# Optimization experiments

Hardware: AMD Instinct MI355X
Metric: run time of the kernel (lower is better)

## Reference

```python
import jax, jax.numpy as jnp
import numpy as np

DEPTH, HEADS, DIM_HEAD = 6, 8, 64
B, N, E = 2, 128, 160
NUM_ATOMS, NF = 100, 127
DIM = NF + 1                 # 128, node feature dim fed to transformer
INNER = HEADS * DIM_HEAD     # 512


def setup_inputs() -> dict:
    key = jax.random.key(0)
    ks = iter(jax.random.split(key, 40))
    f32 = jnp.float32
    def w(shape, scale=0.02):
        return jax.random.normal(next(ks), shape, dtype=f32) * scale
    inp = {
        "indices": jax.random.randint(next(ks), (B, N), 0, NUM_ATOMS),
        "coordinates": jax.random.normal(next(ks), (B, N, 3), dtype=f32),
        "bonds": jax.random.randint(next(ks), (E, 2), 0, N),
        "noise_level": jax.random.uniform(next(ks), (1,), dtype=f32),
        "atom_emb": w((NUM_ATOMS, NF), 1.0),
        "ln1_g": jnp.ones((DEPTH, DIM), f32), "ln1_b": jnp.zeros((DEPTH, DIM), f32),
        "Wq": w((DEPTH, DIM, INNER)), "bq": jnp.zeros((DEPTH, INNER), f32),
        "Wkv": w((DEPTH, DIM, 2 * INNER)), "bkv": jnp.zeros((DEPTH, 2 * INNER), f32),
        "We": w((DEPTH, 3, INNER)), "be": jnp.zeros((DEPTH, INNER), f32),
        "Wo": w((DEPTH, INNER, DIM)), "bo": jnp.zeros((DEPTH, DIM), f32),
        "Wg1": w((DEPTH, 3 * DIM, 1)),
        "ln2_g": jnp.ones((DEPTH, DIM), f32), "ln2_b": jnp.zeros((DEPTH, DIM), f32),
        "W1": w((DEPTH, DIM, 4 * DIM)), "b1": jnp.zeros((DEPTH, 4 * DIM), f32),
        "W2": w((DEPTH, 4 * DIM, DIM)), "b2": jnp.zeros((DEPTH, DIM), f32),
        "Wg2": w((DEPTH, 3 * DIM, 1)),
        "Wlin": w((DIM, 1)), "blin": jnp.zeros((1,), f32),
    }
    return inp


def _ln(x, g, b, eps=1e-5):
    m = jnp.mean(x, -1, keepdims=True)
    v = jnp.mean((x - m) ** 2, -1, keepdims=True)
    return (x - m) * jax.lax.rsqrt(v + eps) * g + b


def _gated_residual(x, res, Wg):
    # gate = sigmoid(Linear([x, res, x-res])); out = x*gate + res*(1-gate)
    gate = jax.nn.sigmoid(jnp.concatenate([x, res, x - res], -1) @ Wg)  # (B,N,1)
    return x * gate + res * (1.0 - gate)


def _forward(indices, bonds, coordinates, noise_level, atom_emb,
             ln1_g, ln1_b, Wq, bq, Wkv, bkv, We, be, Wo, bo, Wg1,
             ln2_g, ln2_b, W1, b1, W2, b2, Wg2, Wlin, blin):
    b, n = indices.shape
    # nodes_embedding: atom embedding + noise-level channel
    noise = jnp.broadcast_to(noise_level.reshape(1, 1, 1).astype(coordinates.dtype), (b, n, 1))
    nodes = jnp.concatenate([atom_emb[indices], noise], -1)  # (B,N,DIM)
    # edges_embedding: vectorized scatter of per-bond coordinate differences
    i, j = bonds[:, 0], bonds[:, 1]
    diff = coordinates[:, i] - coordinates[:, j]             # (B,E,3)
    edges = jnp.zeros((b, n, n, 3), coordinates.dtype)
    edges = edges.at[:, i, j].set(diff).at[:, j, i].set(-diff)

    scale = DIM_HEAD ** -0.5
    for l in range(DEPTH):
        # PreNorm + edge-biased attention (mask is all-ones -> no-op)
        xn = _ln(nodes, ln1_g[l], ln1_b[l])
        q = (xn @ Wq[l] + bq[l]).reshape(b, n, HEADS, DIM_HEAD)
        k, v = jnp.split(xn @ Wkv[l] + bkv[l], 2, -1)
        k = k.reshape(b, n, HEADS, DIM_HEAD)
        v = v.reshape(b, n, HEADS, DIM_HEAD)
        e = (edges @ We[l] + be[l]).reshape(b, n, n, HEADS, DIM_HEAD)
        kk = k[:, None] + e                                   # (B,i,j,H,D)
        vv = v[:, None] + e
        sim = jnp.einsum('bihd,bijhd->bijh', q, kk) * scale
        attn = jax.nn.softmax(sim, axis=2)                    # softmax over j
        out = jnp.einsum('bijh,bijhd->bihd', attn, vv).reshape(b, n, INNER)
        out = out @ Wo[l] + bo[l]
        nodes = _gated_residual(out, nodes, Wg1[l])
        # PreNorm + FeedForward (exact GELU, mult=4) + gated residual
        xn = _ln(nodes, ln2_g[l], ln2_b[l])
        ff = jax.nn.gelu(xn @ W1[l] + b1[l], approximate=False) @ W2[l] + b2[l]
        nodes = _gated_residual(ff, nodes, Wg2[l])
    return jnp.sum(nodes @ Wlin + blin)


def reference(indices, coordinates, bonds, noise_level, atom_emb,
              ln1_g, ln1_b, Wq, bq, Wkv, bkv, We, be, Wo, bo, Wg1,
              ln2_g, ln2_b, W1, b1, W2, b2, Wg2, Wlin, blin):
    return _forward(indices, bonds, coordinates, noise_level, atom_emb,
                    ln1_g, ln1_b, Wq, bq, Wkv, bkv, We, be, Wo, bo, Wg1,
                    ln2_g, ln2_b, W1, b1, W2, b2, Wg2, Wlin, blin)
```

## Files before the change

### kernel.cpp

```cpp
#include <hip/hip_runtime.h>
#include <hip/hip_fp16.h>
#include <math.h>

#define DEPTH 6
#define NN    128
#define EE    160
#define NF    127
#define DIMM  128
#define INNER 512
#define NNODE 256

typedef _Float16 h2f16 __attribute__((ext_vector_type(2)));

#if defined(__has_builtin)
#if __has_builtin(__builtin_amdgcn_fdot2)
#define HAVE_FDOT2 1
#endif
#endif

__device__ __forceinline__ float fdot2f(h2f16 a, h2f16 b, float c) {
#ifdef HAVE_FDOT2
    return __builtin_amdgcn_fdot2(a, b, c, false);
#else
    return c + (float)a.x * (float)b.x + (float)a.y * (float)b.y;
#endif
}

__device__ __forceinline__ void gload16(const void* g, void* l) {
    __builtin_amdgcn_global_load_lds((const __attribute__((address_space(1))) void*)g,
                                     (__attribute__((address_space(3))) void*)l,
                                     16, 0, 0);
}

template <int N>
__device__ __forceinline__ void wait_vm() {
    __builtin_amdgcn_s_waitcnt((0xF << 8) | (7 << 4) | (N & 0xF) | ((N >> 4) << 14));
}
__device__ __forceinline__ void wait_lgkm0() { __builtin_amdgcn_s_waitcnt(0xC07F); }
__device__ __forceinline__ void sbar0() { __builtin_amdgcn_sched_barrier(0); }

__device__ __forceinline__ void stage8c(const char* g, char* lds, int ln) {
#pragma unroll
    for (int i = 0; i < 8; i++)
        gload16(g + i * 1024 + ln * 16, lds + i * 1024);
}
__device__ __forceinline__ void stage8f(const char* g, int rs, char* lds, int ln) {
#pragma unroll
    for (int i = 0; i < 8; i++)
        gload16(g + (size_t)i * rs + ln * 16, lds + i * 1024);
}


template <int NXT>
__device__ __forceinline__ float gemv512v2(const __half* s_xh, float* wbuf,
                                           const char* nextG, int ln) {
    const char* Wb = (const char*)wbuf;
    float4 wa[8], wb[8];
    wait_vm<8>();
#pragma unroll
    for (int i = 0; i < 8; i++) wa[i] = *(const float4*)(Wb + i * 1024 + ln * 16);
    sbar0(); wait_lgkm0(); sbar0();
    if (NXT) { stage8c(nextG, (char*)wbuf, ln); wait_vm<8>(); }
    else     wait_vm<0>();
#pragma unroll
    for (int i = 0; i < 8; i++) wb[i] = *(const float4*)(Wb + 8192 + i * 1024 + ln * 16);
    sbar0(); wait_lgkm0(); sbar0();
    if (NXT) stage8c(nextG + 8192, (char*)wbuf + 8192, ln);
    const float4* X = (const float4*)s_xh;
    float a0 = 0, a1 = 0, a2 = 0, a3 = 0;
#pragma unroll
    for (int i = 0; i < 8; i++) {
        float4 xv = X[i];
        const h2f16* wh = (const h2f16*)&wa[i];
        const h2f16* xh = (const h2f16*)&xv;
        a0 = fdot2f(xh[0], wh[0], a0); a1 = fdot2f(xh[1], wh[1], a1);
        a2 = fdot2f(xh[2], wh[2], a2); a3 = fdot2f(xh[3], wh[3], a3);
    }
#pragma unroll
    for (int i = 0; i < 8; i++) {
        float4 xv = X[8 + i];
        const h2f16* wh = (const h2f16*)&wb[i];
        const h2f16* xh = (const h2f16*)&xv;
        a0 = fdot2f(xh[0], wh[0], a0); a1 = fdot2f(xh[1], wh[1], a1);
        a2 = fdot2f(xh[2], wh[2], a2); a3 = fdot2f(xh[3], wh[3], a3);
    }
    return (a0 + a1) + (a2 + a3);
}

template <int NXT>
__device__ __forceinline__ float gemv128v2(const __half* s_xp, float* wbuf,
                                           const char* nextG, int ln) {
    const char* Wb = (const char*)wbuf;
    const char* Xb = (const char*)s_xp + (ln & 3) * 272;
    float4 wa[8], wb[8];
    wait_vm<8>();
#pragma unroll
    for (int i = 0; i < 8; i++) wa[i] = *(const float4*)(Wb + i * 1024 + ln * 16);
    sbar0(); wait_lgkm0(); sbar0();
    if (NXT) { stage8c(nextG, (char*)wbuf, ln); wait_vm<8>(); }
    else     wait_vm<0>();
#pragma unroll
    for (int i = 0; i < 8; i++) wb[i] = *(const float4*)(Wb + 8192 + i * 1024 + ln * 16);
    sbar0(); wait_lgkm0(); sbar0();
    if (NXT) stage8c(nextG + 8192, (char*)wbuf + 8192, ln);
    float a0 = 0, a1 = 0, a2 = 0, a3 = 0;
#pragma unroll
    for (int i = 0; i < 8; i++) {
        float4 xv = *(const float4*)(Xb + i * 16);
        const h2f16* wh = (const h2f16*)&wa[i];
        const h2f16* xh = (const h2f16*)&xv;
        a0 = fdot2f(xh[0], wh[0], a0); a1 = fdot2f(xh[1], wh[1], a1);
        a2 = fdot2f(xh[2], wh[2], a2); a3 = fdot2f(xh[3], wh[3], a3);
    }
#pragma unroll
    for (int i = 0; i < 8; i++) {
        float4 xv = *(const float4*)(Xb + 128 + i * 16);
        const h2f16* wh = (const h2f16*)&wb[i];
        const h2f16* xh = (const h2f16*)&xv;
        a0 = fdot2f(xh[0], wh[0], a0); a1 = fdot2f(xh[1], wh[1], a1);
        a2 = fdot2f(xh[2], wh[2], a2); a3 = fdot2f(xh[3], wh[3], a3);
    }
    return (a0 + a1) + (a2 + a3);
}

template <int NXT>
__device__ __forceinline__ float4 gemvf32(const float* s_xn, float* wbuf,
                                          const char* nextG, int nrs, int w, int ln) {
    const float4* w4 = (const float4*)wbuf;
    float4 wr[16];
    wait_vm<8>();
#pragma unroll
    for (int r = 0; r < 8; r++) wr[r] = w4[r * 64 + ln];
    sbar0(); wait_lgkm0(); sbar0();
    if (NXT) { stage8f(nextG, nrs, (char*)wbuf, ln); wait_vm<8>(); }
    else     wait_vm<0>();
#pragma unroll
    for (int r = 8; r < 16; r++) wr[r] = w4[r * 64 + ln];
    sbar0(); wait_lgkm0(); sbar0();
    if (NXT) stage8f(nextG + (size_t)8 * nrs, nrs, (char*)wbuf + 8192, ln);
    float4 acc = {0, 0, 0, 0};
#pragma unroll
    for (int r = 0; r < 16; r++) {
        float a = s_xn[w * 16 + r];
        acc.x += a * wr[r].x; acc.y += a * wr[r].y;
        acc.z += a * wr[r].z; acc.w += a * wr[r].w;
    }
    return acc;
}

template <int N>
__device__ __forceinline__ void block_reduce_n(float* vals, float* sbuf) {
#pragma unroll
    for (int off = 32; off > 0; off >>= 1)
#pragma unroll
        for (int q = 0; q < N; q++) vals[q] += __shfl_xor(vals[q], off, 64);
    int wave = threadIdx.x >> 6;
    if ((threadIdx.x & 63) == 0)
#pragma unroll
        for (int q = 0; q < N; q++) sbuf[wave * N + q] = vals[q];
    __syncthreads();
#pragma unroll
    for (int q = 0; q < N; q++) {
        float r = 0.0f;
#pragma unroll
        for (int g = 0; g < 8; g++) r += sbuf[g * N + q];
        vals[q] = r;
    }
    __syncthreads();
}

__device__ __forceinline__ float gelu_exact(float a) {
    return 0.5f * a * (1.0f + erff(a * 0.70710678f));
}

__global__ __launch_bounds__(512, 1) void k_pre(
        const int* indices, const float* coords, const int* bonds, const float* noise,
        const float* atom_emb, const float* ln1_g, const float* ln1_b,
        const float* Wq, const float* bq, const float* Wkv, const float* bkv,
        const float* Wo, const float* W1, const float* W2,
        __half* hWq, __half* hWkv, __half* hWo, __half* hW1, __half* hW2,
        float* nodes, float* qb, __half* hk, __half* hv, float* sedgews,
        const float* blin, float* out) {
    int bn = blockIdx.x;
    int b = bn >> 7, i = bn & 127;
    int t  = threadIdx.x;
    int d  = t & 127;
    bool own = (t < 128);
    int w = t >> 6, ln = t & 63;
    __shared__ float arena[32768];
    __shared__ float scoord[384];
    __shared__ int   sadj[128];
    __shared__ float s_xn[128];
    __shared__ float s_red[48];
    __shared__ float s_part[2048];
    float* wbuf = arena + w * 4096;
    char*  wbufc = (char*)wbuf;

    if (bn == 0 && t == 0) out[0] = 256.0f * blin[0];

    const char* phB[6] = {(const char*)Wq,            (const char*)Wq + 1024,
                          (const char*)Wkv,           (const char*)Wkv + 1024,
                          (const char*)Wkv + 2048,    (const char*)Wkv + 3072};
    const int phRS[6] = {2048, 2048, 4096, 4096, 4096, 4096};

    stage8f(phB[0] + (size_t)(w * 16) * phRS[0], phRS[0], wbufc, ln);
    stage8f(phB[0] + (size_t)(w * 16 + 8) * phRS[0], phRS[0], wbufc + 8192, ln);

    if (t < 3 * NN) scoord[t] = coords[b * 3 * NN + t];
    if (t < NN) sadj[t] = 0;
    __syncthreads();
    if (t < EE) {
        int e0 = bonds[2 * t], e1 = bonds[2 * t + 1];
        if (e0 == i) sadj[e1] = 1;
        if (e1 == i) sadj[e0] = 1;
    }
    __syncthreads();
    if (t < NN) {
        int j = t;
        float msk = sadj[j] ? 1.0f : 0.0f;
        sedgews[bn * 384 + 3 * j + 0] = msk * (scoord[3 * i + 0] - scoord[3 * j + 0]);
        sedgews[bn * 384 + 3 * j + 1] = msk * (scoord[3 * i + 1] - scoord[3 * j + 1]);
        sedgews[bn * 384 + 3 * j + 2] = msk * (scoord[3 * i + 2] - scoord[3 * j + 2]);
    }

    float nd = 0.0f;
    if (own) {
        int idx = indices[bn];
        nd = (d < NF) ? atom_emb[idx * NF + d] : noise[0];
        nodes[bn * DIMM + d] = nd;
    }
    {
        float vals[2] = {own ? nd : 0.0f, own ? nd * nd : 0.0f};
        block_reduce_n<2>(vals, s_red);
        float m   = vals[0] * (1.0f / 128.0f);
        float var = vals[1] * (1.0f / 128.0f) - m * m;
        if (own) s_xn[d] = (nd - m) * rsqrtf(var + 1e-5f) * ln1_g[d] + ln1_b[d];
    }

    for (int u = bn * 512 + t; u < 294912; u += NNODE * 512) {
        int s = u >> 13, within = u & 8191;
        int l = s / 6, m = s % 6;
        const float* src; __half* dst; int ncols, colofs, big;
        if (m == 0)      { src = Wq  + (size_t)l * 65536;  dst = hWq  + (size_t)l * 65536;         ncols = 512;  colofs = 0;   big = 0; }
        else if (m == 1) { src = Wkv + (size_t)l * 131072; dst = hWkv + (size_t)l * 131072;        ncols = 1024; colofs = 0;   big = 0; }
        else if (m == 2) { src = Wkv + (size_t)l * 131072; dst = hWkv + (size_t)l * 131072 + 65536;ncols = 1024; colofs = 512; big = 0; }
        else if (m == 3) { src = W1  + (size_t)l * 65536;  dst = hW1  + (size_t)l * 65536;         ncols = 512;  colofs = 0;   big = 0; }
        else if (m == 4) { src = Wo  + (size_t)l * 65536;  dst = hWo  + (size_t)l * 65536;         ncols = 128;  colofs = 0;   big = 1; }
        else             { src = W2  + (size_t)l * 65536;  dst = hW2  + (size_t)l * 65536;         ncols = 128;  colofs = 0;   big = 1; }
        int rb, col;
        if (!big) { rb = within >> 9; col = within & 511; }
        else      { rb = within >> 7; col = within & 127; }
        int row0 = rb * 8;
        __align__(16) __half tmp[8];
#pragma unroll
        for (int e = 0; e < 8; e++)
            tmp[e] = __float2half(src[(size_t)(row0 + e) * ncols + colofs + col]);
        int dh;
        if (!big) dh = (col >> 6) * 8192 + rb * 512 + (col & 63) * 8;
        else {
            int kq = row0 >> 7, ci = (row0 & 127) >> 3;
            dh = (col >> 4) * 8192 + ci * 512 + ((col & 15) * 4 + kq) * 8;
        }
        *(float4*)&dst[dh] = *(const float4*)tmp;
    }
    __syncthreads();

#define PRE_COMBINE(P)                                                        \
    {                                                                         \
        ((float4*)(s_part + w * 256))[ln] = acc;                              \
        __syncthreads();                                                      \
        if (t < 256) {                                                        \
            float sS = 0.0f;                                                  \
            _Pragma("unroll")                                                 \
            for (int g = 0; g < 8; g++) sS += s_part[g * 256 + t];            \
            int col = ((P) & 1) * 256 + t;                                    \
            if ((P) < 2)      qb[(size_t)bn * INNER + col] = sS + bq[col];    \
            else if ((P) < 4) hk[(size_t)bn * INNER + col] =                  \
                                  __float2half(sS + bkv[col]);                \
            else              hv[(size_t)bn * INNER + col] =                  \
                                  __float2half(sS + bkv[INNER + col]);        \
        }                                                                     \
        __syncthreads();                                                      \
    }

    {
        float4 acc;
        acc = gemvf32<1>(s_xn, wbuf, phB[1] + (size_t)(w * 16) * phRS[1], phRS[1], w, ln);
        PRE_COMBINE(0);
        acc = gemvf32<1>(s_xn, wbuf, phB[2] + (size_t)(w * 16) * phRS[2], phRS[2], w, ln);
        PRE_COMBINE(1);
        acc = gemvf32<1>(s_xn, wbuf, phB[3] + (size_t)(w * 16) * phRS[3], phRS[3], w, ln);
        PRE_COMBINE(2);
        acc = gemvf32<1>(s_xn, wbuf, phB[4] + (size_t)(w * 16) * phRS[4], phRS[4], w, ln);
        PRE_COMBINE(3);
        acc = gemvf32<1>(s_xn, wbuf, phB[5] + (size_t)(w * 16) * phRS[5], phRS[5], w, ln);
        PRE_COMBINE(4);
        acc = gemvf32<0>(s_xn, wbuf, nullptr, 0, w, ln);
        PRE_COMBINE(5);
    }
#undef PRE_COMBINE
}

__global__ __launch_bounds__(512, 1) void k_layer(int l,
        const float* sedgews,
        const float* We, const float* be,
        float* qb, const __half* hkin, const __half* hvin,
        __half* hkout, __half* hvout,
        const __half* hWo, const float* bo, const float* Wg1,
        const float* ln2_g, const float* ln2_b,
        const __half* hW1, const float* b1,
        const __half* hW2, const float* b2,
        const float* Wg2,
        const float* ln1_g, const float* ln1_b,
        const __half* hWq, const float* bq,
        const __half* hWkv, const float* bkv,
        float* nodes, const float* Wlin, float* out) {
    int bn = blockIdx.x;
    int b = bn >> 7;
    int t = threadIdx.x;
    int d = t & 127;
    bool own = (t < 128);
    int w = t >> 6, ln = t & 63;

    __shared__ float arena[32768];
    __shared__ float sedge[384];
    __shared__ float s_l[64];
    __shared__ __align__(16) __half s_aoh[544];
    __shared__ __align__(16) __half s_hh[544];
    __shared__ __align__(16) __half s_xh[128];
    __shared__ float s_x[128];
    __shared__ float s_red[48];
    __shared__ float s_part[4096];
    float* s_o = s_part;
    float* wbuf = arena + w * 4096;

    const char* WoL  = (const char*)hWo + (size_t)l * 131072 + w * 16384;
    const char* W1L  = (const char*)hW1 + (size_t)l * 131072 + w * 16384;
    const char* W2L  = (const char*)hW2 + (size_t)l * 131072 + w * 16384;
    const char* WqnL = (const char*)hWq + (size_t)(l + 1) * 131072 + w * 16384;
    const char* WknL = (const char*)hWkv + (size_t)(l + 1) * 262144 + w * 16384;
    const char* WvnL = (const char*)hWkv + (size_t)(l + 1) * 262144 + 131072 + w * 16384;

    stage8c(WoL, (char*)wbuf, ln);
    stage8c(WoL + 8192, (char*)wbuf + 8192, ln);

    const float4* qR4 = (const float4*)(qb + (size_t)bn * INNER);
    const float4* WeR = (const float4*)(We + (size_t)l * 3 * INNER);
    float4 qa  = qR4[ln * 2],        qz  = qR4[ln * 2 + 1];
    float4 w0a = WeR[ln * 2],        w0z = WeR[ln * 2 + 1];
    float4 w1a = WeR[128 + ln * 2],  w1z = WeR[129 + ln * 2];
    float4 w2a = WeR[256 + ln * 2],  w2z = WeR[257 + ln * 2];
    float4 bea = ((const float4*)(be + (size_t)l * INNER))[ln * 2];
    float4 bez = ((const float4*)(be + (size_t)l * INNER))[ln * 2 + 1];
    float res = own ? nodes[bn * DIMM + d] : 0.0f;
    h2f16 qh0 = {(_Float16)qa.x, (_Float16)qa.y};
    h2f16 qh1 = {(_Float16)qa.z, (_Float16)qa.w};
    h2f16 qh2 = {(_Float16)qz.x, (_Float16)qz.y};
    h2f16 qh3 = {(_Float16)qz.z, (_Float16)qz.w};
    float c = qa.x * bea.x + qa.y * bea.y + qa.z * bea.z + qa.w * bea.w
            + qz.x * bez.x + qz.y * bez.y + qz.z * bez.z + qz.w * bez.w;
    c += __shfl_xor(c, 1, 64); c += __shfl_xor(c, 2, 64); c += __shfl_xor(c, 4, 64);

    if (t < 384) sedge[t] = sedgews[bn * 384 + t];
    __syncthreads();

    const float4* kR = (const float4*)(hkin + (size_t)b * NN * INNER);
    const float4* vR = (const float4*)(hvin + (size_t)b * NN * INNER);
    float l_run = 0.0f, S_nb = 0.0f;
    float4 o0 = {0, 0, 0, 0}, o1 = {0, 0, 0, 0};
    int j0 = w * 16;
#pragma unroll
    for (int base = 0; base < 16; base += 4) {
        float4 kraw[4], vraw[4];
#pragma unroll
        for (int p = 0; p < 4; p++) {
            int j = j0 + base + p;
            kraw[p] = kR[j * 64 + ln];
            vraw[p] = vR[j * 64 + ln];
        }
#pragma unroll
        for (int p = 0; p < 4; p++) {
            int j = j0 + base + p;
            const h2f16* kh = (const h2f16*)&kraw[p];
            float s = fdot2f(qh0, kh[0],
                      fdot2f(qh1, kh[1],
                      fdot2f(qh2, kh[2],
                      fdot2f(qh3, kh[3], 0.0f))));
            float ex = sedge[3 * j], ey = sedge[3 * j + 1], ez = sedge[3 * j + 2];
            bool bonded = (ex != 0.0f) || (ey != 0.0f) || (ez != 0.0f);
            float4 e0, e1;
            if (bonded) {
                e0.x = bea.x + ex * w0a.x + ey * w1a.x + ez * w2a.x;
                e0.y = bea.y + ex * w0a.y + ey * w1a.y + ez * w2a.y;
                e0.z = bea.z + ex * w0a.z + ey * w1a.z + ez * w2a.z;
                e0.w = bea.w + ex * w0a.w + ey * w1a.w + ez * w2a.w;
                e1.x = bez.x + ex * w0z.x + ey * w1z.x + ez * w2z.x;
                e1.y = bez.y + ex * w0z.y + ey * w1z.y + ez * w2z.y;
                e1.z = bez.z + ex * w0z.z + ey * w1z.z + ez * w2z.z;
                e1.w = bez.w + ex * w0z.w + ey * w1z.w + ez * w2z.w;
                s += qa.x * e0.x + qa.y * e0.y + qa.z * e0.z + qa.w * e0.w
                   + qz.x * e1.x + qz.y * e1.y + qz.z * e1.z + qz.w * e1.w;
            }
            s += __shfl_xor(s, 1, 64);
            s += __shfl_xor(s, 2, 64);
            s += __shfl_xor(s, 4, 64);
            if (!bonded) s += c;
            float pp = __expf(s * 0.125f);
            l_run += pp;
            const __half2* vh = (const __half2*)&vraw[p];
            float2 v0 = __half22float2(vh[0]), v1 = __half22float2(vh[1]);
            float2 v2 = __half22float2(vh[2]), v3 = __half22float2(vh[3]);
            o0.x += pp * v0.x; o0.y += pp * v0.y; o0.z += pp * v1.x; o0.w += pp * v1.y;
            o1.x += pp * v2.x; o1.y += pp * v2.y; o1.z += pp * v3.x; o1.w += pp * v3.y;
            if (bonded) {
                o0.x += pp * e0.x; o0.y += pp * e0.y; o0.z += pp * e0.z; o0.w += pp * e0.w;
                o1.x += pp * e1.x; o1.y += pp * e1.y; o1.z += pp * e1.z; o1.w += pp * e1.w;
            } else S_nb += pp;
        }
    }
    o0.x += S_nb * bea.x; o0.y += S_nb * bea.y; o0.z += S_nb * bea.z; o0.w += S_nb * bea.w;
    o1.x += S_nb * bez.x; o1.y += S_nb * bez.y; o1.z += S_nb * bez.z; o1.w += S_nb * bez.w;
    ((float4*)(s_o + w * 512))[ln * 2]     = o0;
    ((float4*)(s_o + w * 512))[ln * 2 + 1] = o1;
    if ((ln & 7) == 0) s_l[w * 8 + (ln >> 3)] = l_run;
    __syncthreads();
    {
        float o = 0.0f;
#pragma unroll
        for (int g = 0; g < 8; g++) o += s_o[g * 512 + t];
        int h = t >> 6;
        float lsum = 0.0f;
#pragma unroll
        for (int g = 0; g < 8; g++) lsum += s_l[g * 8 + h];
        s_aoh[(t >> 7) * 136 + (t & 127)] = __float2half(o / lsum);
    }
    __syncthreads();

    {
        float xo = gemv128v2<1>(s_aoh, wbuf, W1L, ln);
        xo += __shfl_xor(xo, 1, 64);
        xo += __shfl_xor(xo, 2, 64);
        if ((ln & 3) == 0) s_x[w * 16 + (ln >> 2)] = xo;
    }
    __syncthreads();
    float x = own ? s_x[d] + bo[l * DIMM + d] : 0.0f;

    const float* Wg1_l = Wg1 + l * 3 * DIMM;
    float n1;
    {
        float tex = own ? (x * Wg1_l[d] + res * Wg1_l[DIMM + d]
                           + (x - res) * Wg1_l[2 * DIMM + d]) : 0.0f;
        float vals[6] = {tex,
                         own ? x : 0.0f, own ? x * x : 0.0f,
                         own ? x * res : 0.0f,
                         own ? res : 0.0f, own ? res * res : 0.0f};
        block_reduce_n<6>(vals, s_red);
        float g1 = 1.0f / (1.0f + __expf(-vals[0]));
        float sn  = g1 * vals[1] + (1.0f - g1) * vals[4];
        float sn2 = g1 * g1 * vals[2] + 2.0f * g1 * (1.0f - g1) * vals[3]
                  + (1.0f - g1) * (1.0f - g1) * vals[5];
        float m   = sn * (1.0f / 128.0f);
        float var = sn2 * (1.0f / 128.0f) - m * m;
        n1 = x * g1 + res * (1.0f - g1);
        if (own) s_xh[d] = __float2half((n1 - m) * rsqrtf(var + 1e-5f) * ln2_g[l * DIMM + d]
                                        + ln2_b[l * DIMM + d]);
    }
    __syncthreads();

    {
        float a1 = gemv512v2<1>(s_xh, wbuf, W2L, ln);
        int col = w * 64 + ln;
        float ag = gelu_exact(a1 + b1[l * 4 * DIMM + col]);
        s_hh[(col >> 7) * 136 + (col & 127)] = __float2half(ag);
    }
    __syncthreads();

    {
        float yw;
        if (l < DEPTH - 1) yw = gemv128v2<1>(s_hh, wbuf, WqnL, ln);
        else               yw = gemv128v2<0>(s_hh, wbuf, nullptr, ln);
        yw += __shfl_xor(yw, 1, 64);
        yw += __shfl_xor(yw, 2, 64);
        if ((ln & 3) == 0) s_x[w * 16 + (ln >> 2)] = yw;
    }
    __syncthreads();
    float y = own ? s_x[d] + b2[l * DIMM + d] : 0.0f;

    const float* Wg2_l = Wg2 + l * 3 * DIMM;
    if (l < DEPTH - 1) {
        float tex = own ? (y * Wg2_l[d] + n1 * Wg2_l[DIMM + d]
                           + (y - n1) * Wg2_l[2 * DIMM + d]) : 0.0f;
        float vals[6] = {tex,
                         own ? y : 0.0f, own ? y * y : 0.0f,
                         own ? y * n1 : 0.0f,
                         own ? n1 : 0.0f, own ? n1 * n1 : 0.0f};
        block_reduce_n<6>(vals, s_red);
        float g2 = 1.0f / (1.0f + __expf(-vals[0]));
        float sn  = g2 * vals[1] + (1.0f - g2) * vals[4];
        float sn2 = g2 * g2 * vals[2] + 2.0f * g2 * (1.0f - g2) * vals[3]
                  + (1.0f - g2) * (1.0f - g2) * vals[5];
        float m   = sn * (1.0f / 128.0f);
        float var = sn2 * (1.0f / 128.0f) - m * m;
        float n2 = y * g2 + n1 * (1.0f - g2);
        if (own) {
            nodes[bn * DIMM + d] = n2;
            s_xh[d] = __float2half((n2 - m) * rsqrtf(var + 1e-5f) * ln1_g[(l + 1) * DIMM + d]
                                   + ln1_b[(l + 1) * DIMM + d]);
        }
        __syncthreads();

        int col = w * 64 + ln;
        {
            float q = gemv512v2<1>(s_xh, wbuf, WknL, ln);
            qb[(size_t)bn * INNER + col] = q + bq[(l + 1) * INNER + col];
        }
        {
            float kk = gemv512v2<1>(s_xh, wbuf, WvnL, ln);
            hkout[(size_t)bn * INNER + col] =
                __float2half(kk + bkv[(l + 1) * 2 * INNER + col]);
        }
        {
            float vv = gemv512v2<0>(s_xh, wbuf, nullptr, ln);
            hvout[(size_t)bn * INNER + col] =
                __float2half(vv + bkv[(l + 1) * 2 * INNER + INNER + col]);
        }
    } else {
        float wl = own ? Wlin[d] : 0.0f;
        float tex = own ? (y * Wg2_l[d] + n1 * Wg2_l[DIMM + d]
                           + (y - n1) * Wg2_l[2 * DIMM + d]) : 0.0f;
        float vals[3] = {tex, y * wl, n1 * wl};
        block_reduce_n<3>(vals, s_red);
        float g2 = 1.0f / (1.0f + __expf(-vals[0]));
        float tot = g2 * vals[1] + (1.0f - g2) * vals[2];
        if (t == 0) atomicAdd(out, tot);
    }
}

extern "C" void kernel_launch(void* const* d_in, const int* in_sizes, int n_in,
                              void* d_out, int out_size, void* d_ws, size_t ws_size,
                              hipStream_t stream) {
    const int*   indices = (const int*)d_in[0];
    const float* coords  = (const float*)d_in[1];
    const int*   bonds   = (const int*)d_in[2];
    const float* noise   = (const float*)d_in[3];
    const float* atom_emb= (const float*)d_in[4];
    const float* ln1_g   = (const float*)d_in[5];
    const float* ln1_b   = (const float*)d_in[6];
    const float* Wq      = (const float*)d_in[7];
    const float* bq      = (const float*)d_in[8];
    const float* Wkv     = (const float*)d_in[9];
    const float* bkv     = (const float*)d_in[10];
    const float* We      = (const float*)d_in[11];
    const float* be      = (const float*)d_in[12];
    const float* Wo      = (const float*)d_in[13];
    const float* bo      = (const float*)d_in[14];
    const float* Wg1     = (const float*)d_in[15];
    const float* ln2_g   = (const float*)d_in[16];
    const float* ln2_b   = (const float*)d_in[17];
    const float* W1      = (const float*)d_in[18];
    const float* b1      = (const float*)d_in[19];
    const float* W2      = (const float*)d_in[20];
    const float* b2      = (const float*)d_in[21];
    const float* Wg2     = (const float*)d_in[22];
    const float* Wlin    = (const float*)d_in[23];
    const float* blin    = (const float*)d_in[24];

    float*  ws    = (float*)d_ws;
    float*  nodes = ws;
    float*  qb    = nodes + NNODE * DIMM;
    __half* hkb   = (__half*)(qb + NNODE * INNER);
    __half* hvb   = hkb + 2 * NNODE * INNER;
    __half* hWq   = hvb + 2 * NNODE * INNER;
    __half* hWkv  = hWq + DEPTH * DIMM * INNER;
    __half* hWo   = hWkv + DEPTH * DIMM * 2 * INNER;
    __half* hW1   = hWo + DEPTH * INNER * DIMM;
    __half* hW2   = hW1 + DEPTH * DIMM * 4 * DIMM;
    float*  sedgews = (float*)(hW2 + DEPTH * 4 * DIMM * DIMM);

    k_pre<<<NNODE, 512, 0, stream>>>(indices, coords, bonds, noise, atom_emb,
                                     ln1_g, ln1_b, Wq, bq, Wkv, bkv, Wo, W1, W2,
                                     hWq, hWkv, hWo, hW1, hW2,
                                     nodes, qb, hkb, hvb, sedgews, blin, (float*)d_out);
    for (int l = 0; l < DEPTH; l++) {
        const __half* hkin = hkb + (size_t)(l & 1) * NNODE * INNER;
        const __half* hvin = hvb + (size_t)(l & 1) * NNODE * INNER;
        __half* hkout = hkb + (size_t)((l + 1) & 1) * NNODE * INNER;
        __half* hvout = hvb + (size_t)((l + 1) & 1) * NNODE * INNER;
        k_layer<<<NNODE, 512, 0, stream>>>(l, sedgews, We, be,
                                           qb, hkin, hvin, hkout, hvout,
                                           hWo, bo, Wg1, ln2_g, ln2_b, hW1, b1, hW2, b2,
                                           Wg2, ln1_g, ln1_b, hWq, bq, hWkv, bkv,
                                           nodes, Wlin, (float*)d_out);
    }
}
```

Before: 244.5 us.

## Process two nodes per block to reuse staged weights across GEMVs

Each block now handles two query nodes (i and i+64) instead of one, halving the grid to 128 blocks. Every weight tile staged into LDS is dotted against two activation vectors, so per-node weight traffic from global memory and LDS is halved. Reductions, edge setup and the residual/LN logic are duplicated per node within the block. In exchange, fewer blocks occupy the GPU's compute units and per-thread register pressure and serial work per block go up.

```diff
diff --git a/kernel.cpp b/kernel.cpp
--- a/kernel.cpp
+++ b/kernel.cpp
@@ -9,6 +9,7 @@
 #define DIMM  128
 #define INNER 512
 #define NNODE 256
+#define NBLK  128
 
 typedef _Float16 h2f16 __attribute__((ext_vector_type(2)));
 
@@ -52,10 +53,10 @@
 
 
 template <int NXT>
-__device__ __forceinline__ float gemv512v2(const __half* s_xh, float* wbuf,
+__device__ __forceinline__ float2 gemv512d(const __half* s_xh, float* wbuf,
                                            const char* nextG, int ln) {
     const char* Wb = (const char*)wbuf;
-    float4 wa[8], wb[8];
+    float4 wa[8], wb_[8];
     wait_vm<8>();
 #pragma unroll
     for (int i = 0; i < 8; i++) wa[i] = *(const float4*)(Wb + i * 1024 + ln * 16);
@@ -63,36 +64,45 @@
     if (NXT) { stage8c(nextG, (char*)wbuf, ln); wait_vm<8>(); }
     else     wait_vm<0>();
 #pragma unroll
-    for (int i = 0; i < 8; i++) wb[i] = *(const float4*)(Wb + 8192 + i * 1024 + ln * 16);
+    for (int i = 0; i < 8; i++) wb_[i] = *(const float4*)(Wb + 8192 + i * 1024 + ln * 16);
     sbar0(); wait_lgkm0(); sbar0();
     if (NXT) stage8c(nextG + 8192, (char*)wbuf + 8192, ln);
-    const float4* X = (const float4*)s_xh;
-    float a0 = 0, a1 = 0, a2 = 0, a3 = 0;
+    const float4* XA = (const float4*)s_xh;
+    const float4* XB = (const float4*)(s_xh + 128);
+    float aA = 0, aB = 0;
 #pragma unroll
     for (int i = 0; i < 8; i++) {
-        float4 xv = X[i];
+        float4 xvA = XA[i], xvB = XB[i];
         const h2f16* wh = (const h2f16*)&wa[i];
-        const h2f16* xh = (const h2f16*)&xv;
-        a0 = fdot2f(xh[0], wh[0], a0); a1 = fdot2f(xh[1], wh[1], a1);
-        a2 = fdot2f(xh[2], wh[2], a2); a3 = fdot2f(xh[3], wh[3], a3);
+        const h2f16* xa = (const h2f16*)&xvA;
+        const h2f16* xb = (const h2f16*)&xvB;
+        aA = fdot2f(xa[0], wh[0], aA); aA = fdot2f(xa[1], wh[1], aA);
+        aA = fdot2f(xa[2], wh[2], aA); aA = fdot2f(xa[3], wh[3], aA);
+        aB = fdot2f(xb[0], wh[0], aB); aB = fdot2f(xb[1], wh[1], aB);
+        aB = fdot2f(xb[2], wh[2], aB); aB = fdot2f(xb[3], wh[3], aB);
     }
 #pragma unroll
     for (int i = 0; i < 8; i++) {
-        float4 xv = X[8 + i];
-        const h2f16* wh = (const h2f16*)&wb[i];
-        const h2f16* xh = (const h2f16*)&xv;
-        a0 = fdot2f(xh[0], wh[0], a0); a1 = fdot2f(xh[1], wh[1], a1);
-        a2 = fdot2f(xh[2], wh[2], a2); a3 = fdot2f(xh[3], wh[3], a3);
-    }
-    return (a0 + a1) + (a2 + a3);
+        float4 xvA = XA[8 + i], xvB = XB[8 + i];
+        const h2f16* wh = (const h2f16*)&wb_[i];
+        const h2f16* xa = (const h2f16*)&xvA;
+        const h2f16* xb = (const h2f16*)&xvB;
+        aA = fdot2f(xa[0], wh[0], aA); aA = fdot2f(xa[1], wh[1], aA);
+        aA = fdot2f(xa[2], wh[2], aA); aA = fdot2f(xa[3], wh[3], aA);
+        aB = fdot2f(xb[0], wh[0], aB); aB = fdot2f(xb[1], wh[1], aB);
+        aB = fdot2f(xb[2], wh[2], aB); aB = fdot2f(xb[3], wh[3], aB);
+    }
+    return {aA, aB};
 }
 
 template <int NXT>
-__device__ __forceinline__ float gemv128v2(const __half* s_xp, float* wbuf,
-                                           const char* nextG, int ln) {
-    const char* Wb = (const char*)wbuf;
-    const char* Xb = (const char*)s_xp + (ln & 3) * 272;
-    float4 wa[8], wb[8];
+__device__ __forceinline__ float2 gemv128d(const __half* xA, const __half* xB,
+                                           float* wbuf, const char* nextG, int ln) {
+    int kq = ln & 3;
+    const char* Wb  = (const char*)wbuf;
+    const char* XbA = (const char*)xA + kq * 272;
+    const char* XbB = (const char*)xB + kq * 272;
+    float4 wa[8], wb_[8];
     wait_vm<8>();
 #pragma unroll
     for (int i = 0; i < 8; i++) wa[i] = *(const float4*)(Wb + i * 1024 + ln * 16);
@@ -100,32 +110,41 @@
     if (NXT) { stage8c(nextG, (char*)wbuf, ln); wait_vm<8>(); }
     else     wait_vm<0>();
 #pragma unroll
-    for (int i = 0; i < 8; i++) wb[i] = *(const float4*)(Wb + 8192 + i * 1024 + ln * 16);
+    for (int i = 0; i < 8; i++) wb_[i] = *(const float4*)(Wb + 8192 + i * 1024 + ln * 16);
     sbar0(); wait_lgkm0(); sbar0();
     if (NXT) stage8c(nextG + 8192, (char*)wbuf + 8192, ln);
-    float a0 = 0, a1 = 0, a2 = 0, a3 = 0;
+    float aA = 0, aB = 0;
 #pragma unroll
     for (int i = 0; i < 8; i++) {
-        float4 xv = *(const float4*)(Xb + i * 16);
+        float4 xvA = *(const float4*)(XbA + i * 16);
+        float4 xvB = *(const float4*)(XbB + i * 16);
         const h2f16* wh = (const h2f16*)&wa[i];
-        const h2f16* xh = (const h2f16*)&xv;
-        a0 = fdot2f(xh[0], wh[0], a0); a1 = fdot2f(xh[1], wh[1], a1);
-        a2 = fdot2f(xh[2], wh[2], a2); a3 = fdot2f(xh[3], wh[3], a3);
+        const h2f16* xa = (const h2f16*)&xvA;
+        const h2f16* xb = (const h2f16*)&xvB;
+        aA = fdot2f(xa[0], wh[0], aA); aA = fdot2f(xa[1], wh[1], aA);
+        aA = fdot2f(xa[2], wh[2], aA); aA = fdot2f(xa[3], wh[3], aA);
+        aB = fdot2f(xb[0], wh[0], aB); aB = fdot2f(xb[1], wh[1], aB);
+        aB = fdot2f(xb[2], wh[2], aB); aB = fdot2f(xb[3], wh[3], aB);
     }
 #pragma unroll
     for (int i = 0; i < 8; i++) {
-        float4 xv = *(const float4*)(Xb + 128 + i * 16);
-        const h2f16* wh = (const h2f16*)&wb[i];
-        const h2f16* xh = (const h2f16*)&xv;
-        a0 = fdot2f(xh[0], wh[0], a0); a1 = fdot2f(xh[1], wh[1], a1);
-        a2 = fdot2f(xh[2], wh[2], a2); a3 = fdot2f(xh[3], wh[3], a3);
-    }
-    return (a0 + a1) + (a2 + a3);
+        float4 xvA = *(const float4*)(XbA + 128 + i * 16);
+        float4 xvB = *(const float4*)(XbB + 128 + i * 16);
+        const h2f16* wh = (const h2f16*)&wb_[i];
+        const h2f16* xa = (const h2f16*)&xvA;
+        const h2f16* xb = (const h2f16*)&xvB;
+        aA = fdot2f(xa[0], wh[0], aA); aA = fdot2f(xa[1], wh[1], aA);
+        aA = fdot2f(xa[2], wh[2], aA); aA = fdot2f(xa[3], wh[3], aA);
+        aB = fdot2f(xb[0], wh[0], aB); aB = fdot2f(xb[1], wh[1], aB);
+        aB = fdot2f(xb[2], wh[2], aB); aB = fdot2f(xb[3], wh[3], aB);
+    }
+    return {aA, aB};
 }
 
 template <int NXT>
-__device__ __forceinline__ float4 gemvf32(const float* s_xn, float* wbuf,
-                                          const char* nextG, int nrs, int w, int ln) {
+__device__ __forceinline__ void gemvf32d(const float* s_xn, float* wbuf,
+                                         const char* nextG, int nrs, int w, int ln,
+                                         float4& accA, float4& accB) {
     const float4* w4 = (const float4*)wbuf;
     float4 wr[16];
     wait_vm<8>();
@@ -138,14 +157,15 @@
     for (int r = 8; r < 16; r++) wr[r] = w4[r * 64 + ln];
     sbar0(); wait_lgkm0(); sbar0();
     if (NXT) stage8f(nextG + (size_t)8 * nrs, nrs, (char*)wbuf + 8192, ln);
-    float4 acc = {0, 0, 0, 0};
+    accA = {0, 0, 0, 0}; accB = {0, 0, 0, 0};
 #pragma unroll
     for (int r = 0; r < 16; r++) {
-        float a = s_xn[w * 16 + r];
-        acc.x += a * wr[r].x; acc.y += a * wr[r].y;
-        acc.z += a * wr[r].z; acc.w += a * wr[r].w;
-    }
-    return acc;
+        float aA = s_xn[w * 16 + r], aB = s_xn[128 + w * 16 + r];
+        accA.x += aA * wr[r].x; accA.y += aA * wr[r].y;
+        accA.z += aA * wr[r].z; accA.w += aA * wr[r].w;
+        accB.x += aB * wr[r].x; accB.y += aB * wr[r].y;
+        accB.z += aB * wr[r].z; accB.w += aB * wr[r].w;
+    }
 }
 
 template <int N>
@@ -181,22 +201,26 @@
         __half* hWq, __half* hWkv, __half* hWo, __half* hW1, __half* hW2,
         float* nodes, float* qb, __half* hk, __half* hv, float* sedgews,
         const float* blin, float* out) {
-    int bn = blockIdx.x;
-    int b = bn >> 7, i = bn & 127;
+    int blk = blockIdx.x;
+    int b = blk >> 6;
+    int iA = blk & 63, iB = iA + 64;
+    int bnA = b * 128 + iA, bnB = b * 128 + iB;
     int t  = threadIdx.x;
     int d  = t & 127;
-    bool own = (t < 128);
+    bool act = (t < 256);
+    int nodesel = (t >> 7) & 1;
     int w = t >> 6, ln = t & 63;
     __shared__ float arena[32768];
     __shared__ float scoord[384];
-    __shared__ int   sadj[128];
-    __shared__ float s_xn[128];
-    __shared__ float s_red[48];
-    __shared__ float s_part[2048];
+    __shared__ int   sadjA[128];
+    __shared__ int   sadjB[128];
+    __shared__ float s_xn[256];
+    __shared__ float s_red[96];
+    __shared__ float s_part[4096];
     float* wbuf = arena + w * 4096;
     char*  wbufc = (char*)wbuf;
 
-    if (bn == 0 && t == 0) out[0] = 256.0f * blin[0];
+    if (blk == 0 && t == 0) out[0] = 256.0f * blin[0];
 
     const char* phB[6] = {(const char*)Wq,            (const char*)Wq + 1024,
                           (const char*)Wkv,           (const char*)Wkv + 1024,
@@ -207,37 +231,46 @@
     stage8f(phB[0] + (size_t)(w * 16 + 8) * phRS[0], phRS[0], wbufc + 8192, ln);
 
     if (t < 3 * NN) scoord[t] = coords[b * 3 * NN + t];
-    if (t < NN) sadj[t] = 0;
+    if (t < NN) { sadjA[t] = 0; sadjB[t] = 0; }
     __syncthreads();
     if (t < EE) {
         int e0 = bonds[2 * t], e1 = bonds[2 * t + 1];
-        if (e0 == i) sadj[e1] = 1;
-        if (e1 == i) sadj[e0] = 1;
+        if (e0 == iA) sadjA[e1] = 1;
+        if (e1 == iA) sadjA[e0] = 1;
+        if (e0 == iB) sadjB[e1] = 1;
+        if (e1 == iB) sadjB[e0] = 1;
     }
     __syncthreads();
     if (t < NN) {
         int j = t;
-        float msk = sadj[j] ? 1.0f : 0.0f;
-        sedgews[bn * 384 + 3 * j + 0] = msk * (scoord[3 * i + 0] - scoord[3 * j + 0]);
-        sedgews[bn * 384 + 3 * j + 1] = msk * (scoord[3 * i + 1] - scoord[3 * j + 1]);
-        sedgews[bn * 384 + 3 * j + 2] = msk * (scoord[3 * i + 2] - scoord[3 * j + 2]);
+        float mA = sadjA[j] ? 1.0f : 0.0f;
+        float mB = sadjB[j] ? 1.0f : 0.0f;
+        sedgews[bnA * 384 + 3 * j + 0] = mA * (scoord[3 * iA + 0] - scoord[3 * j + 0]);
+        sedgews[bnA * 384 + 3 * j + 1] = mA * (scoord[3 * iA + 1] - scoord[3 * j + 1]);
+        sedgews[bnA * 384 + 3 * j + 2] = mA * (scoord[3 * iA + 2] - scoord[3 * j + 2]);
+        sedgews[bnB * 384 + 3 * j + 0] = mB * (scoord[3 * iB + 0] - scoord[3 * j + 0]);
+        sedgews[bnB * 384 + 3 * j + 1] = mB * (scoord[3 * iB + 1] - scoord[3 * j + 1]);
+        sedgews[bnB * 384 + 3 * j + 2] = mB * (scoord[3 * iB + 2] - scoord[3 * j + 2]);
     }
 
     float nd = 0.0f;
-    if (own) {
-        int idx = indices[bn];
+    if (act) {
+        int idx = indices[nodesel ? bnB : bnA];
         nd = (d < NF) ? atom_emb[idx * NF + d] : noise[0];
-        nodes[bn * DIMM + d] = nd;
+        nodes[(nodesel ? bnB : bnA) * DIMM + d] = nd;
     }
     {
-        float vals[2] = {own ? nd : 0.0f, own ? nd * nd : 0.0f};
-        block_reduce_n<2>(vals, s_red);
-        float m   = vals[0] * (1.0f / 128.0f);
-        float var = vals[1] * (1.0f / 128.0f) - m * m;
-        if (own) s_xn[d] = (nd - m) * rsqrtf(var + 1e-5f) * ln1_g[d] + ln1_b[d];
-    }
-
-    for (int u = bn * 512 + t; u < 294912; u += NNODE * 512) {
+        float vals[4] = {(act && !nodesel) ? nd : 0.0f, (act && !nodesel) ? nd * nd : 0.0f,
+                         (act &&  nodesel) ? nd : 0.0f, (act &&  nodesel) ? nd * nd : 0.0f};
+        block_reduce_n<4>(vals, s_red);
+        float sm = nodesel ? vals[2] : vals[0];
+        float sq = nodesel ? vals[3] : vals[1];
+        float m   = sm * (1.0f / 128.0f);
+        float var = sq * (1.0f / 128.0f) - m * m;
+        if (act) s_xn[t] = (nd - m) * rsqrtf(var + 1e-5f) * ln1_g[d] + ln1_b[d];
+    }
+
+    for (int u = blk * 512 + t; u < 294912; u += NBLK * 512) {
         int s = u >> 13, within = u & 8191;
         int l = s / 6, m = s % 6;
         const float* src; __half* dst; int ncols, colofs, big;
@@ -265,37 +298,40 @@
     }
     __syncthreads();
 
-#define PRE_COMBINE(P)                                                        \
-    {                                                                         \
-        ((float4*)(s_part + w * 256))[ln] = acc;                              \
-        __syncthreads();                                                      \
-        if (t < 256) {                                                        \
-            float sS = 0.0f;                                                  \
-            _Pragma("unroll")                                                 \
-            for (int g = 0; g < 8; g++) sS += s_part[g * 256 + t];            \
-            int col = ((P) & 1) * 256 + t;                                    \
-            if ((P) < 2)      qb[(size_t)bn * INNER + col] = sS + bq[col];    \
-            else if ((P) < 4) hk[(size_t)bn * INNER + col] =                  \
-                                  __float2half(sS + bkv[col]);                \
-            else              hv[(size_t)bn * INNER + col] =                  \
-                                  __float2half(sS + bkv[INNER + col]);        \
-        }                                                                     \
-        __syncthreads();                                                      \
+#define PRE_COMBINE(P)                                                         \
+    {                                                                          \
+        ((float4*)(s_part + w * 256))[ln]        = accA;                       \
+        ((float4*)(s_part + 2048 + w * 256))[ln] = accB;                       \
+        __syncthreads();                                                       \
+        {                                                                      \
+            int nn = t >> 8, tc = t & 255;                                     \
+            float sS = 0.0f;                                                   \
+            _Pragma("unroll")                                                  \
+            for (int g = 0; g < 8; g++) sS += s_part[nn * 2048 + g * 256 + tc];\
+            int col = ((P) & 1) * 256 + tc;                                    \
+            size_t bnX = nn ? (size_t)bnB : (size_t)bnA;                       \
+            if ((P) < 2)      qb[bnX * INNER + col] = sS + bq[col];            \
+            else if ((P) < 4) hk[bnX * INNER + col] =                          \
+                                  __float2half(sS + bkv[col]);                 \
+            else              hv[bnX * INNER + col] =                          \
+                                  __float2half(sS + bkv[INNER + col]);         \
+        }                                                                      \
+        __syncthreads();                                                       \
     }
 
     {
-        float4 acc;
-        acc = gemvf32<1>(s_xn, wbuf, phB[1] + (size_t)(w * 16) * phRS[1], phRS[1], w, ln);
+        float4 accA, accB;
+        gemvf32d<1>(s_xn, wbuf, phB[1] + (size_t)(w * 16) * phRS[1], phRS[1], w, ln, accA, accB);
         PRE_COMBINE(0);
-        acc = gemvf32<1>(s_xn, wbuf, phB[2] + (size_t)(w * 16) * phRS[2], phRS[2], w, ln);
+        gemvf32d<1>(s_xn, wbuf, phB[2] + (size_t)(w * 16) * phRS[2], phRS[2], w, ln, accA, accB);
         PRE_COMBINE(1);
-        acc = gemvf32<1>(s_xn, wbuf, phB[3] + (size_t)(w * 16) * phRS[3], phRS[3], w, ln);
+        gemvf32d<1>(s_xn, wbuf, phB[3] + (size_t)(w * 16) * phRS[3], phRS[3], w, ln, accA, accB);
         PRE_COMBINE(2);
-        acc = gemvf32<1>(s_xn, wbuf, phB[4] + (size_t)(w * 16) * phRS[4], phRS[4], w, ln);
+        gemvf32d<1>(s_xn, wbuf, phB[4] + (size_t)(w * 16) * phRS[4], phRS[4], w, ln, accA, accB);
         PRE_COMBINE(3);
-        acc = gemvf32<1>(s_xn, wbuf, phB[5] + (size_t)(w * 16) * phRS[5], phRS[5], w, ln);
+        gemvf32d<1>(s_xn, wbuf, phB[5] + (size_t)(w * 16) * phRS[5], phRS[5], w, ln, accA, accB);
         PRE_COMBINE(4);
-        acc = gemvf32<0>(s_xn, wbuf, nullptr, 0, w, ln);
+        gemvf32d<0>(s_xn, wbuf, nullptr, 0, w, ln, accA, accB);
         PRE_COMBINE(5);
     }
 #undef PRE_COMBINE
@@ -315,21 +351,24 @@
         const __half* hWq, const float* bq,
         const __half* hWkv, const float* bkv,
         float* nodes, const float* Wlin, float* out) {
-    int bn = blockIdx.x;
-    int b = bn >> 7;
+    int blk = blockIdx.x;
+    int b = blk >> 6;
+    int iA = blk & 63;
+    int bnA = b * 128 + iA, bnB = bnA + 64;
     int t = threadIdx.x;
     int d = t & 127;
-    bool own = (t < 128);
+    bool act = (t < 256);
+    int nodesel = (t >> 7) & 1;
     int w = t >> 6, ln = t & 63;
 
     __shared__ float arena[32768];
-    __shared__ float sedge[384];
-    __shared__ float s_l[64];
-    __shared__ __align__(16) __half s_aoh[544];
-    __shared__ __align__(16) __half s_hh[544];
-    __shared__ __align__(16) __half s_xh[128];
-    __shared__ float s_x[128];
-    __shared__ float s_red[48];
+    __shared__ float sedge[2][384];
+    __shared__ float s_l[2][64];
+    __shared__ __align__(16) __half s_aoh[2][544];
+    __shared__ __align__(16) __half s_hh[2][544];
+    __shared__ __align__(16) __half s_xh[256];
+    __shared__ float s_x[256];
+    __shared__ float s_red[96];
     __shared__ float s_part[4096];
     float* s_o = s_part;
     float* wbuf = arena + w * 4096;
@@ -344,30 +383,42 @@
     stage8c(WoL, (char*)wbuf, ln);
     stage8c(WoL + 8192, (char*)wbuf + 8192, ln);
 
-    const float4* qR4 = (const float4*)(qb + (size_t)bn * INNER);
-    const float4* WeR = (const float4*)(We + (size_t)l * 3 * INNER);
-    float4 qa  = qR4[ln * 2],        qz  = qR4[ln * 2 + 1];
-    float4 w0a = WeR[ln * 2],        w0z = WeR[ln * 2 + 1];
-    float4 w1a = WeR[128 + ln * 2],  w1z = WeR[129 + ln * 2];
-    float4 w2a = WeR[256 + ln * 2],  w2z = WeR[257 + ln * 2];
+    const float4* qR4A = (const float4*)(qb + (size_t)bnA * INNER);
+    const float4* qR4B = (const float4*)(qb + (size_t)bnB * INNER);
+    const float4* WeR  = (const float4*)(We + (size_t)l * 3 * INNER);
+    float4 qaA = qR4A[ln * 2], qzA = qR4A[ln * 2 + 1];
+    float4 qaB = qR4B[ln * 2], qzB = qR4B[ln * 2 + 1];
+    float4 w0a = WeR[ln * 2],       w0z = WeR[ln * 2 + 1];
+    float4 w1a = WeR[128 + ln * 2], w1z = WeR[129 + ln * 2];
+    float4 w2a = WeR[256 + ln * 2], w2z = WeR[257 + ln * 2];
     float4 bea = ((const float4*)(be + (size_t)l * INNER))[ln * 2];
     float4 bez = ((const float4*)(be + (size_t)l * INNER))[ln * 2 + 1];
-    float res = own ? nodes[bn * DIMM + d] : 0.0f;
-    h2f16 qh0 = {(_Float16)qa.x, (_Float16)qa.y};
-    h2f16 qh1 = {(_Float16)qa.z, (_Float16)qa.w};
-    h2f16 qh2 = {(_Float16)qz.x, (_Float16)qz.y};
-    h2f16 qh3 = {(_Float16)qz.z, (_Float16)qz.w};
-    float c = qa.x * bea.x + qa.y * bea.y + qa.z * bea.z + qa.w * bea.w
-            + qz.x * bez.x + qz.y * bez.y + qz.z * bez.z + qz.w * bez.w;
-    c += __shfl_xor(c, 1, 64); c += __shfl_xor(c, 2, 64); c += __shfl_xor(c, 4, 64);
-
-    if (t < 384) sedge[t] = sedgews[bn * 384 + t];
+    float res = act ? nodes[(nodesel ? bnB : bnA) * DIMM + d] : 0.0f;
+    h2f16 qhA0 = {(_Float16)qaA.x, (_Float16)qaA.y};
+    h2f16 qhA1 = {(_Float16)qaA.z, (_Float16)qaA.w};
+    h2f16 qhA2 = {(_Float16)qzA.x, (_Float16)qzA.y};
+    h2f16 qhA3 = {(_Float16)qzA.z, (_Float16)qzA.w};
+    h2f16 qhB0 = {(_Float16)qaB.x, (_Float16)qaB.y};
+    h2f16 qhB1 = {(_Float16)qaB.z, (_Float16)qaB.w};
+    h2f16 qhB2 = {(_Float16)qzB.x, (_Float16)qzB.y};
+    h2f16 qhB3 = {(_Float16)qzB.z, (_Float16)qzB.w};
+    float cA = qaA.x * bea.x + qaA.y * bea.y + qaA.z * bea.z + qaA.w * bea.w
+             + qzA.x * bez.x + qzA.y * bez.y + qzA.z * bez.z + qzA.w * bez.w;
+    float cB = qaB.x * bea.x + qaB.y * bea.y + qaB.z * bea.z + qaB.w * bea.w
+             + qzB.x * bez.x + qzB.y * bez.y + qzB.z * bez.z + qzB.w * bez.w;
+    cA += __shfl_xor(cA, 1, 64); cA += __shfl_xor(cA, 2, 64); cA += __shfl_xor(cA, 4, 64);
+    cB += __shfl_xor(cB, 1, 64); cB += __shfl_xor(cB, 2, 64); cB += __shfl_xor(cB, 4, 64);
+
+    if (t < 384) {
+        sedge[0][t] = sedgews[bnA * 384 + t];
+        sedge[1][t] = sedgews[bnB * 384 + t];
+    }
     __syncthreads();
 
     const float4* kR = (const float4*)(hkin + (size_t)b * NN * INNER);
     const float4* vR = (const float4*)(hvin + (size_t)b * NN * INNER);
-    float l_run = 0.0f, S_nb = 0.0f;
-    float4 o0 = {0, 0, 0, 0}, o1 = {0, 0, 0, 0};
+    float l_runA = 0.0f, S_nbA = 0.0f, l_runB = 0.0f, S_nbB = 0.0f;
+    float4 o0A = {0,0,0,0}, o1A = {0,0,0,0}, o0B = {0,0,0,0}, o1B = {0,0,0,0};
     int j0 = w * 16;
 #pragma unroll
     for (int base = 0; base < 16; base += 4) {
@@ -382,156 +433,224 @@
         for (int p = 0; p < 4; p++) {
             int j = j0 + base + p;
             const h2f16* kh = (const h2f16*)&kraw[p];
-            float s = fdot2f(qh0, kh[0],
-                      fdot2f(qh1, kh[1],
-                      fdot2f(qh2, kh[2],
-                      fdot2f(qh3, kh[3], 0.0f))));
-            float ex = sedge[3 * j], ey = sedge[3 * j + 1], ez = sedge[3 * j + 2];
-            bool bonded = (ex != 0.0f) || (ey != 0.0f) || (ez != 0.0f);
-            float4 e0, e1;
-            if (bonded) {
-                e0.x = bea.x + ex * w0a.x + ey * w1a.x + ez * w2a.x;
-                e0.y = bea.y + ex * w0a.y + ey * w1a.y + ez * w2a.y;
-                e0.z = bea.z + ex * w0a.z + ey * w1a.z + ez * w2a.z;
-                e0.w = bea.w + ex * w0a.w + ey * w1a.w + ez * w2a.w;
-                e1.x = bez.x + ex * w0z.x + ey * w1z.x + ez * w2z.x;
-                e1.y = bez.y + ex * w0z.y + ey * w1z.y + ez * w2z.y;
-                e1.z = bez.z + ex * w0z.z + ey * w1z.z + ez * w2z.z;
-                e1.w = bez.w + ex * w0z.w + ey * w1z.w + ez * w2z.w;
-                s += qa.x * e0.x + qa.y * e0.y + qa.z * e0.z + qa.w * e0.w
-                   + qz.x * e1.x + qz.y * e1.y + qz.z * e1.z + qz.w * e1.w;
+            float sA = fdot2f(qhA0, kh[0], fdot2f(qhA1, kh[1],
+                       fdot2f(qhA2, kh[2], fdot2f(qhA3, kh[3], 0.0f))));
+            float sB = fdot2f(qhB0, kh[0], fdot2f(qhB1, kh[1],
+                       fdot2f(qhB2, kh[2], fdot2f(qhB3, kh[3], 0.0f))));
+            float exA = sedge[0][3 * j], eyA = sedge[0][3 * j + 1], ezA = sedge[0][3 * j + 2];
+            float exB = sedge[1][3 * j], eyB = sedge[1][3 * j + 1], ezB = sedge[1][3 * j + 2];
+            bool bondedA = (exA != 0.0f) || (eyA != 0.0f) || (ezA != 0.0f);
+            bool bondedB = (exB != 0.0f) || (eyB != 0.0f) || (ezB != 0.0f);
+            float4 e0A, e1A, e0B, e1B;
+            if (bondedA) {
+                e0A.x = bea.x + exA * w0a.x + eyA * w1a.x + ezA * w2a.x;
+                e0A.y = bea.y + exA * w0a.y + eyA * w1a.y + ezA * w2a.y;
+                e0A.z = bea.z + exA * w0a.z + eyA * w1a.z + ezA * w2a.z;
+                e0A.w = bea.w + exA * w0a.w + eyA * w1a.w + ezA * w2a.w;
+                e1A.x = bez.x + exA * w0z.x + eyA * w1z.x + ezA * w2z.x;
+                e1A.y = bez.y + exA * w0z.y + eyA * w1z.y + ezA * w2z.y;
+                e1A.z = bez.z + exA * w0z.z + eyA * w1z.z + ezA * w2z.z;
+                e1A.w = bez.w + exA * w0z.w + eyA * w1z.w + ezA * w2z.w;
+                sA += qaA.x * e0A.x + qaA.y * e0A.y + qaA.z * e0A.z + qaA.w * e0A.w
+                    + qzA.x * e1A.x + qzA.y * e1A.y + qzA.z * e1A.z + qzA.w * e1A.w;
             }
-            s += __shfl_xor(s, 1, 64);
-            s += __shfl_xor(s, 2, 64);
-            s += __shfl_xor(s, 4, 64);
-            if (!bonded) s += c;
-            float pp = __expf(s * 0.125f);
-            l_run += pp;
+            if (bondedB) {
+                e0B.x = bea.x + exB * w0a.x + eyB * w1a.x + ezB * w2a.x;
+                e0B.y = bea.y + exB * w0a.y + eyB * w1a.y + ezB * w2a.y;
+                e0B.z = bea.z + exB * w0a.z + eyB * w1a.z + ezB * w2a.z;
+                e0B.w = bea.w + exB * w0a.w + eyB * w1a.w + ezB * w2a.w;
+                e1B.x = bez.x + exB * w0z.x + eyB * w1z.x + ezB * w2z.x;
+                e1B.y = bez.y + exB * w0z.y + eyB * w1z.y + ezB * w2z.y;
+                e1B.z = bez.z + exB * w0z.z + eyB * w1z.z + ezB * w2z.z;
+                e1B.w = bez.w + exB * w0z.w + eyB * w1z.w + ezB * w2z.w;
+                sB += qaB.x * e0B.x + qaB.y * e0B.y + qaB.z * e0B.z + qaB.w * e0B.w
+                    + qzB.x * e1B.x + qzB.y * e1B.y + qzB.z * e1B.z + qzB.w * e1B.w;
+            }
+            sA += __shfl_xor(sA, 1, 64); sA += __shfl_xor(sA, 2, 64); sA += __shfl_xor(sA, 4, 64);
+            sB += __shfl_xor(sB, 1, 64); sB += __shfl_xor(sB, 2, 64); sB += __shfl_xor(sB, 4, 64);
+            if (!bondedA) sA += cA;
+            if (!bondedB) sB += cB;
+            float ppA = __expf(sA * 0.125f);
+            float ppB = __expf(sB * 0.125f);
+            l_runA += ppA; l_runB += ppB;
             const __half2* vh = (const __half2*)&vraw[p];
             float2 v0 = __half22float2(vh[0]), v1 = __half22float2(vh[1]);
             float2 v2 = __half22float2(vh[2]), v3 = __half22float2(vh[3]);
-            o0.x += pp * v0.x; o0.y += pp * v0.y; o0.z += pp * v1.x; o0.w += pp * v1.y;
-            o1.x += pp * v2.x; o1.y += pp * v2.y; o1.z += pp * v3.x; o1.w += pp * v3.y;
-            if (bonded) {
-                o0.x += pp * e0.x; o0.y += pp * e0.y; o0.z += pp * e0.z; o0.w += pp * e0.w;
-                o1.x += pp * e1.x; o1.y += pp * e1.y; o1.z += pp * e1.z; o1.w += pp * e1.w;
-            } else S_nb += pp;
-        }
-    }
-    o0.x += S_nb * bea.x; o0.y += S_nb * bea.y; o0.z += S_nb * bea.z; o0.w += S_nb * bea.w;
-    o1.x += S_nb * bez.x; o1.y += S_nb * bez.y; o1.z += S_nb * bez.z; o1.w += S_nb * bez.w;
-    ((float4*)(s_o + w * 512))[ln * 2]     = o0;
-    ((float4*)(s_o + w * 512))[ln * 2 + 1] = o1;
-    if ((ln & 7) == 0) s_l[w * 8 + (ln >> 3)] = l_run;
-    __syncthreads();
+            o0A.x += ppA * v0.x; o0A.y += ppA * v0.y; o0A.z += ppA * v1.x; o0A.w += ppA * v1.y;
+            o1A.x += ppA * v2.x; o1A.y += ppA * v2.y; o1A.z += ppA * v3.x; o1A.w += ppA * v3.y;
+            o0B.x += ppB * v0.x; o0B.y += ppB * v0.y; o0B.z += ppB * v1.x; o0B.w += ppB * v1.y;
+            o1B.x += ppB * v2.x; o1B.y += ppB * v2.y; o1B.z += ppB * v3.x; o1B.w += ppB * v3.y;
+            if (bondedA) {
+                o0A.x += ppA * e0A.x; o0A.y += ppA * e0A.y; o0A.z += ppA * e0A.z; o0A.w += ppA * e0A.w;
+                o1A.x += ppA * e1A.x; o1A.y += ppA * e1A.y; o1A.z += ppA * e1A.z; o1A.w += ppA * e1A.w;
+            } else S_nbA += ppA;
+            if (bondedB) {
+                o0B.x += ppB * e0B.x; o0B.y += ppB * e0B.y; o0B.z += ppB * e0B.z; o0B.w += ppB * e0B.w;
+                o1B.x += ppB * e1B.x; o1B.y += ppB * e1B.y; o1B.z += ppB * e1B.z; o1B.w += ppB * e1B.w;
+            } else S_nbB += ppB;
+        }
+    }
+    o0A.x += S_nbA * bea.x; o0A.y += S_nbA * bea.y; o0A.z += S_nbA * bea.z; o0A.w += S_nbA * bea.w;
+    o1A.x += S_nbA * bez.x; o1A.y += S_nbA * bez.y; o1A.z += S_nbA * bez.z; o1A.w += S_nbA * bez.w;
+    o0B.x += S_nbB * bea.x; o0B.y += S_nbB * bea.y; o0B.z += S_nbB * bea.z; o0B.w += S_nbB * bea.w;
+    o1B.x += S_nbB * bez.x; o1B.y += S_nbB * bez.y; o1B.z += S_nbB * bez.z; o1B.w += S_nbB * bez.w;
+
+    ((float4*)(s_o + w * 512))[ln * 2]     = o0A;
+    ((float4*)(s_o + w * 512))[ln * 2 + 1] = o1A;
+    if ((ln & 7) == 0) {
+        s_l[0][w * 8 + (ln >> 3)] = l_runA;
+        s_l[1][w * 8 + (ln >> 3)] = l_runB;
+    }
+    __syncthreads();
+    float oaccA = 0.0f, lsumA = 0.0f;
     {
-        float o = 0.0f;
-#pragma unroll
-        for (int g = 0; g < 8; g++) o += s_o[g * 512 + t];
+#pragma unroll
+        for (int g = 0; g < 8; g++) oaccA += s_o[g * 512 + t];
         int h = t >> 6;
-        float lsum = 0.0f;
-#pragma unroll
-        for (int g = 0; g < 8; g++) lsum += s_l[g * 8 + h];
-        s_aoh[(t >> 7) * 136 + (t & 127)] = __float2half(o / lsum);
-    }
-    __syncthreads();
-
+#pragma unroll
+        for (int g = 0; g < 8; g++) lsumA += s_l[0][g * 8 + h];
+    }
+    __syncthreads();
+    ((float4*)(s_o + w * 512))[ln * 2]     = o0B;
+    ((float4*)(s_o + w * 512))[ln * 2 + 1] = o1B;
+    __syncthreads();
     {
-        float xo = gemv128v2<1>(s_aoh, wbuf, W1L, ln);
-        xo += __shfl_xor(xo, 1, 64);
-        xo += __shfl_xor(xo, 2, 64);
-        if ((ln & 3) == 0) s_x[w * 16 + (ln >> 2)] = xo;
-    }
-    __syncthreads();
-    float x = own ? s_x[d] + bo[l * DIMM + d] : 0.0f;
+        float oaccB = 0.0f, lsumB = 0.0f;
+#pragma unroll
+        for (int g = 0; g < 8; g++) oaccB += s_o[g * 512 + t];
+        int h = t >> 6;
+#pragma unroll
+        for (int g = 0; g < 8; g++) lsumB += s_l[1][g * 8 + h];
+        int idx = (t >> 7) * 136 + (t & 127);
+        s_aoh[0][idx] = __float2half(oaccA / lsumA);
+        s_aoh[1][idx] = __float2half(oaccB / lsumB);
+    }
+    __syncthreads();
+
+    {
+        float2 xo = gemv128d<1>(s_aoh[0], s_aoh[1], wbuf, W1L, ln);
+        xo.x += __shfl_xor(xo.x, 1, 64); xo.x += __shfl_xor(xo.x, 2, 64);
+        xo.y += __shfl_xor(xo.y, 1, 64); xo.y += __shfl_xor(xo.y, 2, 64);
+        if ((ln & 3) == 0) {
+            s_x[w * 16 + (ln >> 2)]       = xo.x;
+            s_x[128 + w * 16 + (ln >> 2)] = xo.y;
+        }
+    }
+    __syncthreads();
+    float x = act ? s_x[t] + bo[l * DIMM + d] : 0.0f;
 
     const float* Wg1_l = Wg1 + l * 3 * DIMM;
     float n1;
     {
-        float tex = own ? (x * Wg1_l[d] + res * Wg1_l[DIMM + d]
+        float tex = act ? (x * Wg1_l[d] + res * Wg1_l[DIMM + d]
                            + (x - res) * Wg1_l[2 * DIMM + d]) : 0.0f;
-        float vals[6] = {tex,
-                         own ? x : 0.0f, own ? x * x : 0.0f,
-                         own ? x * res : 0.0f,
-                         own ? res : 0.0f, own ? res * res : 0.0f};
-        block_reduce_n<6>(vals, s_red);
-        float g1 = 1.0f / (1.0f + __expf(-vals[0]));
-        float sn  = g1 * vals[1] + (1.0f - g1) * vals[4];
-        float sn2 = g1 * g1 * vals[2] + 2.0f * g1 * (1.0f - g1) * vals[3]
-                  + (1.0f - g1) * (1.0f - g1) * vals[5];
+        float v6[6] = {tex, x, x * x, x * res, res, res * res};
+        float vals[12];
+#pragma unroll
+        for (int q = 0; q < 6; q++) {
+            vals[q]     = (act && !nodesel) ? v6[q] : 0.0f;
+            vals[6 + q] = (act &&  nodesel) ? v6[q] : 0.0f;
+        }
+        block_reduce_n<12>(vals, s_red);
+        const float* vv = vals + 6 * nodesel;
+        float g1 = 1.0f / (1.0f + __expf(-vv[0]));
+        float sn  = g1 * vv[1] + (1.0f - g1) * vv[4];
+        float sn2 = g1 * g1 * vv[2] + 2.0f * g1 * (1.0f - g1) * vv[3]
+                  + (1.0f - g1) * (1.0f - g1) * vv[5];
         float m   = sn * (1.0f / 128.0f);
         float var = sn2 * (1.0f / 128.0f) - m * m;
         n1 = x * g1 + res * (1.0f - g1);
-        if (own) s_xh[d] = __float2half((n1 - m) * rsqrtf(var + 1e-5f) * ln2_g[l * DIMM + d]
+        if (act) s_xh[t] = __float2half((n1 - m) * rsqrtf(var + 1e-5f) * ln2_g[l * DIMM + d]
                                         + ln2_b[l * DIMM + d]);
     }
     __syncthreads();
 
     {
-        float a1 = gemv512v2<1>(s_xh, wbuf, W2L, ln);
+        float2 a1 = gemv512d<1>(s_xh, wbuf, W2L, ln);
         int col = w * 64 + ln;
-        float ag = gelu_exact(a1 + b1[l * 4 * DIMM + col]);
-        s_hh[(col >> 7) * 136 + (col & 127)] = __float2half(ag);
+        float bb = b1[l * 4 * DIMM + col];
+        int idx = (col >> 7) * 136 + (col & 127);
+        s_hh[0][idx] = __float2half(gelu_exact(a1.x + bb));
+        s_hh[1][idx] = __float2half(gelu_exact(a1.y + bb));
     }
     __syncthreads();
 
     {
-        float yw;
-        if (l < DEPTH - 1) yw = gemv128v2<1>(s_hh, wbuf, WqnL, ln);
-        else               yw = gemv128v2<0>(s_hh, wbuf, nullptr, ln);
-        yw += __shfl_xor(yw, 1, 64);
-        yw += __shfl_xor(yw, 2, 64);
-        if ((ln & 3) == 0) s_x[w * 16 + (ln >> 2)] = yw;
-    }
-    __syncthreads();
-    float y = own ? s_x[d] + b2[l * DIMM + d] : 0.0f;
+        float2 yw;
+        if (l < DEPTH - 1) yw = gemv128d<1>(s_hh[0], s_hh[1], wbuf, WqnL, ln);
+        else               yw = gemv128d<0>(s_hh[0], s_hh[1], wbuf, nullptr, ln);
+        yw.x += __shfl_xor(yw.x, 1, 64); yw.x += __shfl_xor(yw.x, 2, 64);
+        yw.y += __shfl_xor(yw.y, 1, 64); yw.y += __shfl_xor(yw.y, 2, 64);
+        if ((ln & 3) == 0) {
+            s_x[w * 16 + (ln >> 2)]       = yw.x;
+            s_x[128 + w * 16 + (ln >> 2)] = yw.y;
+        }
+    }
+    __syncthreads();
+    float y = act ? s_x[t] + b2[l * DIMM + d] : 0.0f;
 
     const float* Wg2_l = Wg2 + l * 3 * DIMM;
     if (l < DEPTH - 1) {
-        float tex = own ? (y * Wg2_l[d] + n1 * Wg2_l[DIMM + d]
+        float tex = act ? (y * Wg2_l[d] + n1 * Wg2_l[DIMM + d]
                            + (y - n1) * Wg2_l[2 * DIMM + d]) : 0.0f;
-        float vals[6] = {tex,
-                         own ? y : 0.0f, own ? y * y : 0.0f,
-                         own ? y * n1 : 0.0f,
-                         own ? n1 : 0.0f, own ? n1 * n1 : 0.0f};
-        block_reduce_n<6>(vals, s_red);
-        float g2 = 1.0f / (1.0f + __expf(-vals[0]));
-        float sn  = g2 * vals[1] + (1.0f - g2) * vals[4];
-        float sn2 = g2 * g2 * vals[2] + 2.0f * g2 * (1.0f - g2) * vals[3]
-                  + (1.0f - g2) * (1.0f - g2) * vals[5];
+        float v6[6] = {tex, y, y * y, y * n1, n1, n1 * n1};
+        float vals[12];
+#pragma unroll
+        for (int q = 0; q < 6; q++) {
+            vals[q]     = (act && !nodesel) ? v6[q] : 0.0f;
+            vals[6 + q] = (act &&  nodesel) ? v6[q] : 0.0f;
+        }
+        block_reduce_n<12>(vals, s_red);
+        const float* vv = vals + 6 * nodesel;
+        float g2 = 1.0f / (1.0f + __expf(-vv[0]));
+        float sn  = g2 * vv[1] + (1.0f - g2) * vv[4];
+        float sn2 = g2 * g2 * vv[2] + 2.0f * g2 * (1.0f - g2) * vv[3]
+                  + (1.0f - g2) * (1.0f - g2) * vv[5];
         float m   = sn * (1.0f / 128.0f);
         float var = sn2 * (1.0f / 128.0f) - m * m;
         float n2 = y * g2 + n1 * (1.0f - g2);
-        if (own) {
-            nodes[bn * DIMM + d] = n2;
-            s_xh[d] = __float2half((n2 - m) * rsqrtf(var + 1e-5f) * ln1_g[(l + 1) * DIMM + d]
+        if (act) {
+            nodes[(nodesel ? bnB : bnA) * DIMM + d] = n2;
+            s_xh[t] = __float2half((n2 - m) * rsqrtf(var + 1e-5f) * ln1_g[(l + 1) * DIMM + d]
                                    + ln1_b[(l + 1) * DIMM + d]);
         }
         __syncthreads();
 
         int col = w * 64 + ln;
         {
-            float q = gemv512v2<1>(s_xh, wbuf, WknL, ln);
-            qb[(size_t)bn * INNER + col] = q + bq[(l + 1) * INNER + col];
+            float2 q = gemv512d<1>(s_xh, wbuf, WknL, ln);
+            float bb = bq[(l + 1) * INNER + col];
+            qb[(size_t)bnA * INNER + col] = q.x + bb;
+            qb[(size_t)bnB * INNER + col] = q.y + bb;
         }
         {
-            float kk = gemv512v2<1>(s_xh, wbuf, WvnL, ln);
-            hkout[(size_t)bn * INNER + col] =
-                __float2half(kk + bkv[(l + 1) * 2 * INNER + col]);
+            float2 kk = gemv512d<1>(s_xh, wbuf, WvnL, ln);
+            float bb = bkv[(l + 1) * 2 * INNER + col];
+            hkout[(size_t)bnA * INNER + col] = __float2half(kk.x + bb);
+            hkout[(size_t)bnB * INNER + col] = __float2half(kk.y + bb);
         }
         {
-            float vv = gemv512v2<0>(s_xh, wbuf, nullptr, ln);
-            hvout[(size_t)bn * INNER + col] =
-                __float2half(vv + bkv[(l + 1) * 2 * INNER + INNER + col]);
+            float2 vv2 = gemv512d<0>(s_xh, wbuf, nullptr, ln);
+            float bb = bkv[(l + 1) * 2 * INNER + INNER + col];
+            hvout[(size_t)bnA * INNER + col] = __float2half(vv2.x + bb);
+            hvout[(size_t)bnB * INNER + col] = __float2half(vv2.y + bb);
         }
     } else {
-        float wl = own ? Wlin[d] : 0.0f;
-        float tex = own ? (y * Wg2_l[d] + n1 * Wg2_l[DIMM + d]
+        float wl = act ? Wlin[d] : 0.0f;
+        float tex = act ? (y * Wg2_l[d] + n1 * Wg2_l[DIMM + d]
                            + (y - n1) * Wg2_l[2 * DIMM + d]) : 0.0f;
-        float vals[3] = {tex, y * wl, n1 * wl};
-        block_reduce_n<3>(vals, s_red);
-        float g2 = 1.0f / (1.0f + __expf(-vals[0]));
-        float tot = g2 * vals[1] + (1.0f - g2) * vals[2];
+        float v3[3] = {tex, y * wl, n1 * wl};
+        float vals[6];
+#pragma unroll
+        for (int q = 0; q < 3; q++) {
+            vals[q]     = (act && !nodesel) ? v3[q] : 0.0f;
+            vals[3 + q] = (act &&  nodesel) ? v3[q] : 0.0f;
+        }
+        block_reduce_n<6>(vals, s_red);
+        float g2A = 1.0f / (1.0f + __expf(-vals[0]));
+        float g2B = 1.0f / (1.0f + __expf(-vals[3]));
+        float tot = g2A * vals[1] + (1.0f - g2A) * vals[2]
+                  + g2B * vals[4] + (1.0f - g2B) * vals[5];
         if (t == 0) atomicAdd(out, tot);
     }
 }
@@ -577,19 +696,19 @@
     __half* hW2   = hW1 + DEPTH * DIMM * 4 * DIMM;
     float*  sedgews = (float*)(hW2 + DEPTH * 4 * DIMM * DIMM);
 
-    k_pre<<<NNODE, 512, 0, stream>>>(indices, coords, bonds, noise, atom_emb,
-                                     ln1_g, ln1_b, Wq, bq, Wkv, bkv, Wo, W1, W2,
-                                     hWq, hWkv, hWo, hW1, hW2,
-                                     nodes, qb, hkb, hvb, sedgews, blin, (float*)d_out);
+    k_pre<<<NBLK, 512, 0, stream>>>(indices, coords, bonds, noise, atom_emb,
+                                    ln1_g, ln1_b, Wq, bq, Wkv, bkv, Wo, W1, W2,
+                                    hWq, hWkv, hWo, hW1, hW2,
+                                    nodes, qb, hkb, hvb, sedgews, blin, (float*)d_out);
     for (int l = 0; l < DEPTH; l++) {
         const __half* hkin = hkb + (size_t)(l & 1) * NNODE * INNER;
         const __half* hvin = hvb + (size_t)(l & 1) * NNODE * INNER;
         __half* hkout = hkb + (size_t)((l + 1) & 1) * NNODE * INNER;
         __half* hvout = hvb + (size_t)((l + 1) & 1) * NNODE * INNER;
-        k_layer<<<NNODE, 512, 0, stream>>>(l, sedgews, We, be,
-                                           qb, hkin, hvin, hkout, hvout,
-                                           hWo, bo, Wg1, ln2_g, ln2_b, hW1, b1, hW2, b2,
-                                           Wg2, ln1_g, ln1_b, hWq, bq, hWkv, bkv,
-                                           nodes, Wlin, (float*)d_out);
-    }
-}
+        k_layer<<<NBLK, 512, 0, stream>>>(l, sedgews, We, be,
+                                          qb, hkin, hvin, hkout, hvout,
+                                          hWo, bo, Wg1, ln2_g, ln2_b, hW1, b1, hW2, b2,
+                                          Wg2, ln1_g, ln1_b, hWq, bq, hWkv, bkv,
+                                          nodes, Wlin, (float*)d_out);
+    }
+}
```

New measurement: 276.7 us. +13.2%, slower.
